# Kernel tuning notes

Measured on AMD Instinct MI355X. Metric: run time of the kernel, lower is better.

## Reference

```python
import jax, jax.numpy as jnp
import numpy as np
import math

DIM = 512
B, T, H, W = 1, 8, 64, 64


def setup_inputs() -> dict:
    key = jax.random.key(0)
    k0, k1, k2 = jax.random.split(key, 3)
    x = jax.random.normal(k0, (B, DIM, T, H, W), dtype=jnp.float32)
    gamma = jnp.ones((DIM,), jnp.float32)                      # RMS_norm gamma (viewed as flat vector)
    w_qkv = jax.random.normal(k1, (3 * DIM, DIM), jnp.float32) * 0.02  # conv1x1 weight (out, in)
    b_qkv = jnp.zeros((3 * DIM,), jnp.float32)
    w_proj = jax.random.normal(k2, (DIM, DIM), jnp.float32) * 0.02     # zero-init in torch; random for a meaningful baseline
    b_proj = jnp.zeros((DIM,), jnp.float32)
    return dict(x=x, gamma=gamma, w_qkv=w_qkv, b_qkv=b_qkv, w_proj=w_proj, b_proj=b_proj)


def reference(x, gamma, w_qkv, b_qkv, w_proj, b_proj):
    b, c, t, h, w = x.shape
    xt = jnp.transpose(x, (0, 2, 3, 4, 1))          # [b, t, h, w, c]
    identity = xt
    y = xt.reshape(b * t, h, w, c)
    # RMS_norm: L2 norm over channels (last dim), clamped, scaled by sqrt(c)*gamma
    norm = jnp.clip(jnp.linalg.norm(y, axis=-1, keepdims=True), 1e-12, None)
    y = y / norm * (c ** 0.5) * gamma
    # 1x1 conv QKV as GEMM over channels
    qkv = jnp.einsum('bhwc,oc->bhwo', y, w_qkv) + b_qkv        # [bt, h, w, 3c]
    qkv = qkv.reshape(b * t, h * w, 1, 3 * c)                  # nh=1 per source rearrange
    q, k, v = jnp.split(qkv, 3, axis=-1)                       # each [bt, hw, 1, c]
    scale = 1.0 / math.sqrt(c)
    # NOTE: hw sits in the batch position (faithful to source); seq len = nh = 1
    attn = jnp.einsum('bsnc,bsmc->bsnm', q, k) * scale         # [bt, hw, 1, 1]
    attn = jax.nn.softmax(attn, axis=-1)                       # trivially 1.0
    o = jnp.einsum('bsnm,bsmc->bsnc', attn, v)                 # == v
    o = o.reshape(b * t, h, w, c)
    o = jnp.einsum('bhwc,oc->bhwo', o, w_proj) + b_proj        # 1x1 proj conv
    o = o.reshape(b, t, h, w, c)
    out = jnp.transpose(o + identity, (0, 4, 1, 2, 3))         # back to [b, c, t, h, w]
    return out
```

## Files before the change

kernel.cpp:

```cpp
#include <hip/hip_runtime.h>

typedef unsigned short ushort_t;
typedef __attribute__((ext_vector_type(8))) short short8;
typedef __attribute__((ext_vector_type(4))) float f32x4;

#define DIMC 512
#define PN   32768
#define SQRTC 22.627416997969522f

__device__ __forceinline__ ushort_t f2bf(float f) {
  unsigned int u = __float_as_uint(f);
  unsigned int r = u + 0x7fffu + ((u >> 16) & 1u);
  return (ushort_t)(r >> 16);
}

__global__ __launch_bounds__(256) void k_cast(const float* __restrict__ a,
                                              ushort_t* __restrict__ b) {
  int i = (blockIdx.x * 256 + threadIdx.x) * 4;
  float4 v = *(const float4*)(a + i);
  ushort_t o[4] = {f2bf(v.x), f2bf(v.y), f2bf(v.z), f2bf(v.w)};
  *(uint2*)(b + i) = *(const uint2*)o;
}

__global__ __launch_bounds__(64) void k_wvt(const float* __restrict__ wqkv,
                                            ushort_t* __restrict__ WvT) {
  int c = blockIdx.x;
  int k8 = threadIdx.x * 8;
  ushort_t tmp[8];
#pragma unroll
  for (int j = 0; j < 8; ++j)
    tmp[j] = f2bf(wqkv[(long)(1024 + k8 + j) * DIMC + c]);
  *(uint4*)(WvT + (long)c * DIMC + k8) = *(const uint4*)tmp;
}

__global__ __launch_bounds__(256) void k_fb(const float* __restrict__ wp,
                                            const float* __restrict__ bqkv,
                                            const float* __restrict__ bproj,
                                            float* __restrict__ fb) {
  int wave = threadIdx.x >> 6;
  int lane = threadIdx.x & 63;
  int o = blockIdx.x * 4 + wave;
  float part = 0.f;
#pragma unroll
  for (int i = 0; i < 8; ++i) {
    int k = lane + i * 64;
    part += wp[o * DIMC + k] * bqkv[1024 + k];
  }
  for (int off = 32; off; off >>= 1) part += __shfl_down(part, off, 64);
  if (lane == 0) fb[o] = part + bproj[o];
}

__global__ __launch_bounds__(256) void k_prep_x(const float* __restrict__ x,
                                                ushort_t* __restrict__ xT,
                                                float* __restrict__ s) {
  __shared__ ushort_t xt[64 * 264];
  __shared__ float red[16 * 64];
  int tid = threadIdx.x;
  long p0 = (long)blockIdx.x * 64;
  int cg = tid >> 4;
  int p4 = (tid & 15) * 4;
  float ss0 = 0.f, ss1 = 0.f, ss2 = 0.f, ss3 = 0.f;
  for (int half = 0; half < 2; ++half) {
    __syncthreads();
#pragma unroll 4
    for (int pass = 0; pass < 16; ++pass) {
      int cl = pass * 16 + cg;
      int c = half * 256 + cl;
      float4 v = *(const float4*)(x + (long)c * PN + p0 + p4);
      xt[(p4 + 0) * 264 + cl] = f2bf(v.x);
      xt[(p4 + 1) * 264 + cl] = f2bf(v.y);
      xt[(p4 + 2) * 264 + cl] = f2bf(v.z);
      xt[(p4 + 3) * 264 + cl] = f2bf(v.w);
      ss0 += v.x * v.x; ss1 += v.y * v.y; ss2 += v.z * v.z; ss3 += v.w * v.w;
    }
    __syncthreads();
#pragma unroll
    for (int i = 0; i < 8; ++i) {
      int chunk = tid + i * 256;
      int r = chunk >> 5;
      int c8 = (chunk & 31) * 8;
      uint4 v = *(const uint4*)(&xt[r * 264 + c8]);
      *(uint4*)(xT + (p0 + r) * DIMC + half * 256 + c8) = v;
    }
  }
  red[cg * 64 + p4 + 0] = ss0;
  red[cg * 64 + p4 + 1] = ss1;
  red[cg * 64 + p4 + 2] = ss2;
  red[cg * 64 + p4 + 3] = ss3;
  __syncthreads();
  if (tid < 64) {
    float t = 0.f;
#pragma unroll
    for (int g = 0; g < 16; ++g) t += red[g * 64 + tid];
    s[p0 + tid] = SQRTC / fmaxf(sqrtf(t), 1e-12f);
  }
}

template <int EPI>
__global__ __launch_bounds__(256) void k_gemm_f(
    const ushort_t* __restrict__ A,
    const ushort_t* __restrict__ BT,
    long Nstr,
    void* __restrict__ Cv,
    const float* __restrict__ gamma,
    const float* __restrict__ xid,
    const float* __restrict__ fb,
    const float* __restrict__ s) {
  __shared__ ushort_t As[128 * 64];
  __shared__ ushort_t Bs[128 * 64];
  int tid = threadIdx.x;
  int p0 = blockIdx.x * 128;
  int o0 = blockIdx.y * 128;
  int wave = tid >> 6, lane = tid & 63;
  int wo = (wave & 1) * 64, wp = (wave >> 1) * 64;
  int q = lane >> 4, ln = lane & 15;

  f32x4 zero = {0.f, 0.f, 0.f, 0.f};
  f32x4 acc[4][4];
#pragma unroll
  for (int i = 0; i < 4; ++i)
#pragma unroll
    for (int j = 0; j < 4; ++j) acc[i][j] = zero;

  int sr = tid >> 3;
  int sc = tid & 7;
  const ushort_t* Ag = A + (long)(o0 + sr) * DIMC + sc * 8;
  const ushort_t* Bg = BT + (long)(p0 + sr) * DIMC + sc * 8;

  for (int kc = 0; kc < DIMC; kc += 64) {
    __syncthreads();
#pragma unroll
    for (int it = 0; it < 4; ++it) {
      int r = sr + it * 32;
      uint4 va = *(const uint4*)(Ag + (long)it * 32 * DIMC + kc);
      uint4 vb = *(const uint4*)(Bg + (long)it * 32 * DIMC + kc);
      int sw = ((sc ^ (r & 7)) * 8);
      *(uint4*)(&As[r * 64 + sw]) = va;
      *(uint4*)(&Bs[r * 64 + sw]) = vb;
    }
    __syncthreads();
#pragma unroll
    for (int ks = 0; ks < 2; ++ks) {
      int cch = ks * 4 + q;
      short8 af[4], bf[4];
#pragma unroll
      for (int mi = 0; mi < 4; ++mi) {
        int row = wo + mi * 16 + ln;
        af[mi] = *(const short8*)(&As[row * 64 + ((cch ^ (row & 7)) * 8)]);
      }
#pragma unroll
      for (int ni = 0; ni < 4; ++ni) {
        int row = wp + ni * 16 + ln;
        bf[ni] = *(const short8*)(&Bs[row * 64 + ((cch ^ (row & 7)) * 8)]);
      }
#pragma unroll
      for (int mi = 0; mi < 4; ++mi)
#pragma unroll
        for (int ni = 0; ni < 4; ++ni)
          acc[mi][ni] = __builtin_amdgcn_mfma_f32_16x16x32_bf16(af[mi], bf[ni], acc[mi][ni], 0, 0, 0);
    }
  }

#pragma unroll
  for (int mi = 0; mi < 4; ++mi) {
    int obase = o0 + wo + mi * 16 + q * 4;
#pragma unroll
    for (int ni = 0; ni < 4; ++ni) {
      int p = p0 + wp + ni * 16 + ln;
      if (EPI == 0) {
        ushort_t* C = (ushort_t*)Cv;
        float g = gamma[p];
#pragma unroll
        for (int r = 0; r < 4; ++r)
          C[(long)(obase + r) * Nstr + p] = f2bf(acc[mi][ni][r] * g);
      } else {
        float* C = (float*)Cv;
        float sv = s[p];
#pragma unroll
        for (int r = 0; r < 4; ++r) {
          int o = obase + r;
          C[(long)o * Nstr + p] = xid[(long)o * Nstr + p] + fb[o] + sv * acc[mi][ni][r];
        }
      }
    }
  }
}

extern "C" void kernel_launch(void* const* d_in, const int* in_sizes, int n_in,
                              void* d_out, int out_size, void* d_ws, size_t ws_size,
                              hipStream_t stream) {
  const float* x     = (const float*)d_in[0];
  const float* gamma = (const float*)d_in[1];
  const float* wqkv  = (const float*)d_in[2];
  const float* bqkv  = (const float*)d_in[3];
  const float* wproj = (const float*)d_in[4];
  const float* bproj = (const float*)d_in[5];

  char* ws = (char*)d_ws;
  ushort_t* Mp  = (ushort_t*)(ws);
  ushort_t* wpb = (ushort_t*)(ws + 524288);
  ushort_t* WvT = (ushort_t*)(ws + 1048576);
  float*    fb  = (float*)(ws + 1572864);
  float*    s   = (float*)(ws + 1576960);
  ushort_t* xT  = (ushort_t*)(ws + 2097152);

  k_cast<<<dim3(256), dim3(256), 0, stream>>>(wproj, wpb);
  k_wvt<<<dim3(512), dim3(64), 0, stream>>>(wqkv, WvT);
  k_fb<<<dim3(128), dim3(256), 0, stream>>>(wproj, bqkv, bproj, fb);
  k_prep_x<<<dim3(512), dim3(256), 0, stream>>>(x, xT, s);
  k_gemm_f<0><<<dim3(4, 4), dim3(256), 0, stream>>>(
      wpb, WvT, 512, Mp, gamma, nullptr, nullptr, nullptr);
  k_gemm_f<1><<<dim3(256, 4), dim3(256), 0, stream>>>(
      Mp, xT, PN, d_out, nullptr, x, fb, s);
}
```

Before: 176.8 us.

## Fuse x transpose, RMS norm, and projection GEMM into a single kernel

Drops the separate prep kernel that wrote a transposed bf16 copy of x and a per-pixel scale to workspace. A new fused kernel loads a 64-pixel tile of x across all 512 channels and computes the norm scale. It stores the bf16 tile swizzled in shared memory and runs the full 512x64 GEMM per block, with weights read straight from global memory. This removes the xT round trip and one launch, but uses 64KB of LDS per block and repeatedly reads the A operand (Mp) from global/L2 without shared-memory staging.

```diff
diff --git a/kernel.cpp b/kernel.cpp
--- a/kernel.cpp
+++ b/kernel.cpp
@@ -50,62 +50,11 @@
   if (lane == 0) fb[o] = part + bproj[o];
 }
 
-__global__ __launch_bounds__(256) void k_prep_x(const float* __restrict__ x,
-                                                ushort_t* __restrict__ xT,
-                                                float* __restrict__ s) {
-  __shared__ ushort_t xt[64 * 264];
-  __shared__ float red[16 * 64];
-  int tid = threadIdx.x;
-  long p0 = (long)blockIdx.x * 64;
-  int cg = tid >> 4;
-  int p4 = (tid & 15) * 4;
-  float ss0 = 0.f, ss1 = 0.f, ss2 = 0.f, ss3 = 0.f;
-  for (int half = 0; half < 2; ++half) {
-    __syncthreads();
-#pragma unroll 4
-    for (int pass = 0; pass < 16; ++pass) {
-      int cl = pass * 16 + cg;
-      int c = half * 256 + cl;
-      float4 v = *(const float4*)(x + (long)c * PN + p0 + p4);
-      xt[(p4 + 0) * 264 + cl] = f2bf(v.x);
-      xt[(p4 + 1) * 264 + cl] = f2bf(v.y);
-      xt[(p4 + 2) * 264 + cl] = f2bf(v.z);
-      xt[(p4 + 3) * 264 + cl] = f2bf(v.w);
-      ss0 += v.x * v.x; ss1 += v.y * v.y; ss2 += v.z * v.z; ss3 += v.w * v.w;
-    }
-    __syncthreads();
-#pragma unroll
-    for (int i = 0; i < 8; ++i) {
-      int chunk = tid + i * 256;
-      int r = chunk >> 5;
-      int c8 = (chunk & 31) * 8;
-      uint4 v = *(const uint4*)(&xt[r * 264 + c8]);
-      *(uint4*)(xT + (p0 + r) * DIMC + half * 256 + c8) = v;
-    }
-  }
-  red[cg * 64 + p4 + 0] = ss0;
-  red[cg * 64 + p4 + 1] = ss1;
-  red[cg * 64 + p4 + 2] = ss2;
-  red[cg * 64 + p4 + 3] = ss3;
-  __syncthreads();
-  if (tid < 64) {
-    float t = 0.f;
-#pragma unroll
-    for (int g = 0; g < 16; ++g) t += red[g * 64 + tid];
-    s[p0 + tid] = SQRTC / fmaxf(sqrtf(t), 1e-12f);
-  }
-}
-
-template <int EPI>
-__global__ __launch_bounds__(256) void k_gemm_f(
+__global__ __launch_bounds__(256) void k_gemm_w(
     const ushort_t* __restrict__ A,
     const ushort_t* __restrict__ BT,
-    long Nstr,
-    void* __restrict__ Cv,
-    const float* __restrict__ gamma,
-    const float* __restrict__ xid,
-    const float* __restrict__ fb,
-    const float* __restrict__ s) {
+    ushort_t* __restrict__ C,
+    const float* __restrict__ gamma) {
   __shared__ ushort_t As[128 * 64];
   __shared__ ushort_t Bs[128 * 64];
   int tid = threadIdx.x;
@@ -167,20 +116,112 @@
 #pragma unroll
     for (int ni = 0; ni < 4; ++ni) {
       int p = p0 + wp + ni * 16 + ln;
-      if (EPI == 0) {
-        ushort_t* C = (ushort_t*)Cv;
-        float g = gamma[p];
-#pragma unroll
-        for (int r = 0; r < 4; ++r)
-          C[(long)(obase + r) * Nstr + p] = f2bf(acc[mi][ni][r] * g);
-      } else {
-        float* C = (float*)Cv;
-        float sv = s[p];
-#pragma unroll
-        for (int r = 0; r < 4; ++r) {
-          int o = obase + r;
-          C[(long)o * Nstr + p] = xid[(long)o * Nstr + p] + fb[o] + sv * acc[mi][ni][r];
-        }
+      float g = gamma[p];
+#pragma unroll
+      for (int r = 0; r < 4; ++r)
+        C[(long)(obase + r) * DIMC + p] = f2bf(acc[mi][ni][r] * g);
+    }
+  }
+}
+
+__global__ __launch_bounds__(512, 4) void k_fused(
+    const float* __restrict__ x,
+    const ushort_t* __restrict__ Mp,
+    const float* __restrict__ fb,
+    float* __restrict__ out) {
+  __shared__ ushort_t xs[8 * 64 * 64];
+  __shared__ float red[32 * 65];
+  __shared__ float s_sh[64];
+  int tid = threadIdx.x;
+  long p0 = (long)blockIdx.x * 64;
+
+  int pl4 = (tid & 15) * 4;
+  int kq  = tid >> 4;
+  float ss0 = 0.f, ss1 = 0.f, ss2 = 0.f, ss3 = 0.f;
+#pragma unroll
+  for (int sw = 0; sw < 4; ++sw) {
+    int k4 = kq * 4 + sw * 128;
+    const float* xp = x + (long)k4 * PN + p0 + pl4;
+    float4 v0 = *(const float4*)(xp);
+    float4 v1 = *(const float4*)(xp + PN);
+    float4 v2 = *(const float4*)(xp + 2 * PN);
+    float4 v3 = *(const float4*)(xp + 3 * PN);
+    ss0 += v0.x * v0.x + v1.x * v1.x + v2.x * v2.x + v3.x * v3.x;
+    ss1 += v0.y * v0.y + v1.y * v1.y + v2.y * v2.y + v3.y * v3.y;
+    ss2 += v0.z * v0.z + v1.z * v1.z + v2.z * v2.z + v3.z * v3.z;
+    ss3 += v0.w * v0.w + v1.w * v1.w + v2.w * v2.w + v3.w * v3.w;
+    ushort_t t0[4] = {f2bf(v0.x), f2bf(v1.x), f2bf(v2.x), f2bf(v3.x)};
+    ushort_t t1[4] = {f2bf(v0.y), f2bf(v1.y), f2bf(v2.y), f2bf(v3.y)};
+    ushort_t t2[4] = {f2bf(v0.z), f2bf(v1.z), f2bf(v2.z), f2bf(v3.z)};
+    ushort_t t3[4] = {f2bf(v0.w), f2bf(v1.w), f2bf(v2.w), f2bf(v3.w)};
+    char* base = (char*)xs + (k4 >> 6) * 8192;
+    int ch  = (k4 >> 3) & 7;
+    int sub = (k4 & 7) * 2;
+    *(uint2*)(base + (pl4 + 0) * 128 + ((ch ^ ((pl4 + 0) & 7)) * 16) + sub) = *(const uint2*)t0;
+    *(uint2*)(base + (pl4 + 1) * 128 + ((ch ^ ((pl4 + 1) & 7)) * 16) + sub) = *(const uint2*)t1;
+    *(uint2*)(base + (pl4 + 2) * 128 + ((ch ^ ((pl4 + 2) & 7)) * 16) + sub) = *(const uint2*)t2;
+    *(uint2*)(base + (pl4 + 3) * 128 + ((ch ^ ((pl4 + 3) & 7)) * 16) + sub) = *(const uint2*)t3;
+  }
+  red[kq * 65 + pl4 + 0] = ss0;
+  red[kq * 65 + pl4 + 1] = ss1;
+  red[kq * 65 + pl4 + 2] = ss2;
+  red[kq * 65 + pl4 + 3] = ss3;
+  __syncthreads();
+  if (tid < 64) {
+    float t = 0.f;
+#pragma unroll
+    for (int g = 0; g < 32; ++g) t += red[g * 65 + tid];
+    s_sh[tid] = SQRTC / fmaxf(sqrtf(t), 1e-12f);
+  }
+  __syncthreads();
+
+  int wave = tid >> 6, lane = tid & 63;
+  int q = lane >> 4, ln = lane & 15;
+  int wo = wave * 64;
+  f32x4 zero = {0.f, 0.f, 0.f, 0.f};
+  f32x4 acc[4][4];
+#pragma unroll
+  for (int i = 0; i < 4; ++i)
+#pragma unroll
+    for (int j = 0; j < 4; ++j) acc[i][j] = zero;
+
+  const ushort_t* Ap = Mp + (long)wo * DIMC;
+#pragma unroll 2
+  for (int kb = 0; kb < 8; ++kb) {
+    const char* bbase = (const char*)xs + kb * 8192;
+#pragma unroll
+    for (int ks = 0; ks < 2; ++ks) {
+      int cch = ks * 4 + q;
+      int kk = kb * 64 + cch * 8;
+      short8 af[4], bf[4];
+#pragma unroll
+      for (int mi = 0; mi < 4; ++mi)
+        af[mi] = *(const short8*)(Ap + (long)(mi * 16 + ln) * DIMC + kk);
+#pragma unroll
+      for (int ni = 0; ni < 4; ++ni) {
+        int row = ni * 16 + ln;
+        bf[ni] = *(const short8*)(bbase + row * 128 + ((cch ^ (row & 7)) * 16));
+      }
+#pragma unroll
+      for (int mi = 0; mi < 4; ++mi)
+#pragma unroll
+        for (int ni = 0; ni < 4; ++ni)
+          acc[mi][ni] = __builtin_amdgcn_mfma_f32_16x16x32_bf16(af[mi], bf[ni], acc[mi][ni], 0, 0, 0);
+    }
+  }
+
+#pragma unroll
+  for (int mi = 0; mi < 4; ++mi) {
+    int obase = wo + mi * 16 + q * 4;
+#pragma unroll
+    for (int ni = 0; ni < 4; ++ni) {
+      int plocal = ni * 16 + ln;
+      long p = p0 + plocal;
+      float sv = s_sh[plocal];
+#pragma unroll
+      for (int r = 0; r < 4; ++r) {
+        int o = obase + r;
+        out[(long)o * PN + p] = x[(long)o * PN + p] + fb[o] + sv * acc[mi][ni][r];
       }
     }
   }
@@ -201,15 +242,10 @@
   ushort_t* wpb = (ushort_t*)(ws + 524288);
   ushort_t* WvT = (ushort_t*)(ws + 1048576);
   float*    fb  = (float*)(ws + 1572864);
-  float*    s   = (float*)(ws + 1576960);
-  ushort_t* xT  = (ushort_t*)(ws + 2097152);
 
   k_cast<<<dim3(256), dim3(256), 0, stream>>>(wproj, wpb);
   k_wvt<<<dim3(512), dim3(64), 0, stream>>>(wqkv, WvT);
   k_fb<<<dim3(128), dim3(256), 0, stream>>>(wproj, bqkv, bproj, fb);
-  k_prep_x<<<dim3(512), dim3(256), 0, stream>>>(x, xT, s);
-  k_gemm_f<0><<<dim3(4, 4), dim3(256), 0, stream>>>(
-      wpb, WvT, 512, Mp, gamma, nullptr, nullptr, nullptr);
-  k_gemm_f<1><<<dim3(256, 4), dim3(256), 0, stream>>>(
-      Mp, xT, PN, d_out, nullptr, x, fb, s);
-}
+  k_gemm_w<<<dim3(4, 4), dim3(256), 0, stream>>>(wpb, WvT, Mp, gamma);
+  k_fused<<<dim3(512), dim3(512), 0, stream>>>(x, Mp, fb, (float*)d_out);
+}
```

Result: no change. 174.8 us (-1.1%).
